# Optimization experiments

Hardware: AMD Instinct MI355X
Metric: run time of the kernel (lower is better)

Reference implementation:

```python
import jax, jax.numpy as jnp
import numpy as np

GROUPS = 4
PPG = 16  # kv_channels // groups = 64 // 4
Q_CH = 256
KV_CH = 64


def setup_inputs() -> dict:
    key = jax.random.key(0)
    ks = jax.random.split(key, 7)
    N, T, L = 4, 64, 64
    q = jax.random.normal(ks[0], (N, L, L, Q_CH), dtype=jnp.float32)
    kv = jax.random.normal(ks[1], (N, T, L, L, KV_CH), dtype=jnp.float32)
    # torch nn.Linear weights, stored pre-transposed so y = x @ W
    s_q = 1.0 / np.sqrt(Q_CH)
    s_kv = 1.0 / np.sqrt(KV_CH)
    Wq = jax.random.uniform(ks[2], (Q_CH, KV_CH), jnp.float32, -s_q, s_q)
    Wk = jax.random.uniform(ks[3], (KV_CH, KV_CH), jnp.float32, -s_kv, s_kv)
    Wv = jax.random.uniform(ks[4], (KV_CH, KV_CH), jnp.float32, -s_kv, s_kv)
    Wout = jax.random.uniform(ks[5], (KV_CH, Q_CH), jnp.float32, -s_kv, s_kv)
    b_out = jax.random.uniform(ks[6], (Q_CH,), jnp.float32, -s_kv, s_kv)
    return {"q": q, "kv": kv, "Wq": Wq, "Wk": Wk, "Wv": Wv, "Wout": Wout, "b_out": b_out}


def reference(q, kv, Wq, Wk, Wv, Wout, b_out):
    N, L, _, _ = q.shape
    T = kv.shape[1]
    qh = (q @ Wq).reshape(N, L, L, GROUPS, PPG)                 # nijgc
    kh = (kv @ Wk).reshape(N, T, L, L, GROUPS, PPG)             # ntijgc
    vh = (kv @ Wv).reshape(N, T, L, L, GROUPS, PPG)             # ntijgc
    scale = 1.0 / jnp.sqrt(jnp.float32(PPG))
    attn = jnp.einsum('nijgc,ntijgc->ntijg', qh, kh) * scale    # scores over T per pixel
    attn = jax.nn.softmax(attn, axis=1)
    x = jnp.einsum('ntijg,ntijgc->nijgc', attn, vh).reshape(N, L, L, KV_CH)
    return x @ Wout + b_out
```

## Files before the change

### kernel.cpp

```cpp
#include <hip/hip_runtime.h>

typedef short short8 __attribute__((ext_vector_type(8)));
typedef short short4v __attribute__((ext_vector_type(4)));
typedef float f32x4 __attribute__((ext_vector_type(4)));

__device__ __forceinline__ float bf2f(unsigned short u) {
  union { unsigned int i; float f; } v; v.i = ((unsigned int)u) << 16; return v.f;
}
__device__ __forceinline__ unsigned short f2bf(float f) {
  unsigned int x = __float_as_uint(f);
  unsigned int r = (x + 0x7fffu + ((x >> 16) & 1u)) >> 16;
  return (unsigned short)r;
}

__global__ __launch_bounds__(256) void prep_kernel(
    const float* __restrict__ Wq, const float* __restrict__ Wk,
    const float* __restrict__ Wv, const float* __restrict__ Wout,
    unsigned short* __restrict__ Afrag, unsigned short* __restrict__ WVOfrag) {
  const int b = blockIdx.x, tid = threadIdx.x;
  if (b < 256) {
    const int p = b, g = tid >> 6, d = tid & 63;
    float s = 0.f;
#pragma unroll
    for (int c = 0; c < 16; ++c)
      s += Wq[p * 64 + g * 16 + c] * Wk[d * 64 + g * 16 + c];
    s *= 0.25f;
    const int n = g * 64 + d, k = p;
    Afrag[(size_t)(k >> 5) * 8192 + n * 32 + (k & 31)] = f2bf(s);
  } else {
    const int row = b - 256, g = row >> 6, d = row & 63, q = tid;
    float s = 0.f;
#pragma unroll
    for (int c = 0; c < 16; ++c)
      s += Wv[d * 64 + g * 16 + c] * Wout[(g * 16 + c) * 256 + q];
    WVOfrag[(size_t)(row >> 5) * 8192 + q * 32 + (row & 31)] = f2bf(s);
  }
}

template <int MODE>
__global__ __launch_bounds__(256) void gemm256_kernel(
    const void* __restrict__ Xv, const unsigned short* __restrict__ Wfrag,
    void* __restrict__ Outv, const float* __restrict__ bias) {
  __shared__ unsigned short A_s[32 * 40];
  const int tid = threadIdx.x;
  const int m0 = blockIdx.x * 32;
  const int w = tid >> 6, lane = tid & 63;
  const int m_l = lane & 15, quad = lane >> 4;
  const int nt0 = (w & 1) * 8, m16 = (w >> 1) * 16;
  const int srow = tid >> 3, sc4 = (tid & 7) * 4;

  f32x4 acc[8];
#pragma unroll
  for (int i = 0; i < 8; ++i) acc[i] = (f32x4){0.f, 0.f, 0.f, 0.f};

  for (int ks = 0; ks < 8; ++ks) {
    if (MODE == 0) {
      const float* X = (const float*)Xv;
      float4 x = *(const float4*)(X + (size_t)(m0 + srow) * 256 + ks * 32 + sc4);
      short4v vv;
      vv[0] = (short)f2bf(x.x); vv[1] = (short)f2bf(x.y);
      vv[2] = (short)f2bf(x.z); vv[3] = (short)f2bf(x.w);
      *(short4v*)&A_s[srow * 40 + sc4] = vv;
    } else {
      const unsigned short* X = (const unsigned short*)Xv;
      uint2 xv = *(const uint2*)(X + (size_t)(m0 + srow) * 256 + ks * 32 + sc4);
      *(uint2*)&A_s[srow * 40 + sc4] = xv;
    }
    __syncthreads();
    short8 a = *(const short8*)&A_s[(m16 + m_l) * 40 + quad * 8];
#pragma unroll
    for (int j = 0; j < 8; ++j) {
      const unsigned short* bp =
          Wfrag + ((size_t)ks * 256 + (nt0 + j) * 16 + m_l) * 32 + quad * 8;
      short8 bfr = *(const short8*)bp;
      acc[j] = __builtin_amdgcn_mfma_f32_16x16x32_bf16(a, bfr, acc[j], 0, 0, 0);
    }
    __syncthreads();
  }
  const int row0 = m0 + m16 + quad * 4;
#pragma unroll
  for (int j = 0; j < 8; ++j) {
    const int col = (nt0 + j) * 16 + m_l;
    if (MODE == 0) {
      unsigned short* Out = (unsigned short*)Outv;
#pragma unroll
      for (int r = 0; r < 4; ++r)
        Out[(size_t)(row0 + r) * 256 + col] = f2bf(acc[j][r]);
    } else {
      float* Out = (float*)Outv;
      const float bb = bias[col];
#pragma unroll
      for (int r = 0; r < 4; ++r)
        Out[(size_t)(row0 + r) * 256 + col] = acc[j][r] + bb;
    }
  }
}

__global__ __launch_bounds__(256) void attn_kernel(
    const float* __restrict__ kv, const unsigned short* __restrict__ qk,
    unsigned short* __restrict__ yout) {
  __shared__ float kv_s[64 * 68];
  __shared__ float p2[256];
  __shared__ float yst[64 * 20];
  float* s_lds = yst;

  const int pixel = blockIdx.x;
  const int tid = threadIdx.x;
  const int t = tid >> 2, q4 = tid & 3;

  const unsigned short* qkb = qk + ((size_t)pixel << 8);
  uint4 qa[4], qb[4];
#pragma unroll
  for (int g = 0; g < 4; ++g) {
    const uint4* qp = (const uint4*)(qkb + g * 64 + q4 * 16);
    qa[g] = qp[0]; qb[g] = qp[1];
  }
  const float* kvb =
      kv + ((size_t)(pixel >> 12) << 24) + (size_t)(pixel & 4095) * 64;
  const float4* kp = (const float4*)(kvb + (size_t)t * 262144 + q4 * 16);
  float4 k0 = kp[0], k1 = kp[1], k2 = kp[2], k3 = kp[3];

  float4* ksw = (float4*)&kv_s[t * 68 + q4 * 16];
  ksw[0] = k0; ksw[1] = k1; ksw[2] = k2; ksw[3] = k3;
  const float kvr[16] = {k0.x, k0.y, k0.z, k0.w, k1.x, k1.y, k1.z, k1.w,
                         k2.x, k2.y, k2.z, k2.w, k3.x, k3.y, k3.z, k3.w};

  float sg[4];
#pragma unroll
  for (int g = 0; g < 4; ++g) {
    const unsigned int uu[8] = {qa[g].x, qa[g].y, qa[g].z, qa[g].w,
                                qb[g].x, qb[g].y, qb[g].z, qb[g].w};
    float acc = 0.f;
#pragma unroll
    for (int i = 0; i < 8; ++i) {
      acc = fmaf(kvr[2 * i],     bf2f((unsigned short)(uu[i] & 0xffffu)), acc);
      acc = fmaf(kvr[2 * i + 1], bf2f((unsigned short)(uu[i] >> 16)),     acc);
    }
    sg[g] = acc;
  }
#pragma unroll
  for (int g = 0; g < 4; ++g) {
    float v = sg[g];
    v += __shfl_xor(v, 1);
    v += __shfl_xor(v, 2);
    sg[g] = v;
  }
  s_lds[q4 * 65 + t] = sg[q4];
  __syncthreads();

  {
    const int g = tid >> 6, tt = tid & 63;
    float x = s_lds[g * 65 + tt];
    float m = x;
#pragma unroll
    for (int o = 32; o > 0; o >>= 1) m = fmaxf(m, __shfl_xor(m, o));
    float e = __expf(x - m);
    float ssum = e;
#pragma unroll
    for (int o = 32; o > 0; o >>= 1) ssum += __shfl_xor(ssum, o);
    p2[tt * 4 + g] = e / ssum;
  }
  __syncthreads();

  {
    const int tq = tid >> 6, d = tid & 63;
    float a0 = 0.f, a1 = 0.f, a2 = 0.f, a3 = 0.f;
#pragma unroll
    for (int i = 0; i < 16; ++i) {
      const int t2 = tq * 16 + i;
      const float kvv = kv_s[t2 * 68 + d];
      const float4 pv = *(const float4*)&p2[t2 * 4];
      a0 = fmaf(pv.x, kvv, a0);
      a1 = fmaf(pv.y, kvv, a1);
      a2 = fmaf(pv.z, kvv, a2);
      a3 = fmaf(pv.w, kvv, a3);
    }
    __syncthreads();
    yst[d * 20 + 0 + tq] = a0;
    yst[d * 20 + 4 + tq] = a1;
    yst[d * 20 + 8 + tq] = a2;
    yst[d * 20 + 12 + tq] = a3;
  }
  __syncthreads();

  {
    const int g = tid >> 6, d = tid & 63;
    const float4 v = *(const float4*)&yst[d * 20 + g * 4];
    yout[((size_t)pixel << 8) + g * 64 + d] = f2bf(v.x + v.y + v.z + v.w);
  }
}

extern "C" void kernel_launch(void* const* d_in, const int* in_sizes, int n_in,
                              void* d_out, int out_size, void* d_ws,
                              size_t ws_size, hipStream_t stream) {
  const float* q    = (const float*)d_in[0];
  const float* kv   = (const float*)d_in[1];
  const float* Wq   = (const float*)d_in[2];
  const float* Wk   = (const float*)d_in[3];
  const float* Wv   = (const float*)d_in[4];
  const float* Wout = (const float*)d_in[5];
  const float* bout = (const float*)d_in[6];

  unsigned short* ws      = (unsigned short*)d_ws;
  unsigned short* Afrag   = ws;
  unsigned short* WVOfrag = ws + 65536;
  unsigned short* qk_ws   = ws + 131072;
  unsigned short* y_ws    = ws + 131072 + 4194304;

  hipLaunchKernelGGL(prep_kernel, dim3(512), dim3(256), 0, stream,
                     Wq, Wk, Wv, Wout, Afrag, WVOfrag);
  hipLaunchKernelGGL((gemm256_kernel<0>), dim3(512), dim3(256), 0, stream,
                     (const void*)q, Afrag, (void*)qk_ws, (const float*)nullptr);
  hipLaunchKernelGGL(attn_kernel, dim3(16384), dim3(256), 0, stream,
                     kv, qk_ws, y_ws);
  hipLaunchKernelGGL((gemm256_kernel<1>), dim3(512), dim3(256), 0, stream,
                     (const void*)y_ws, WVOfrag, d_out, bout);
}
```

Measured before the change: 422.6 us.

## Restructure attention into per-row blocks with streamed async KV loads and online softmax

The attention kernel now runs one workgroup per (batch, row) of 64 pixels instead of one per pixel. Each thread owns one pixel-group pair and loops over T. KV tiles are streamed into a triple-buffered LDS ring with global_load_lds async copies, and scores and the weighted sum are accumulated in a single pass. The goal is contiguous, overlapped KV reads and far fewer tiny workgroups with their repeated barriers. The cost is only 256 workgroups at one wave group per CU, heavy register use, and an exp taken without subtracting the max, which can overflow for large scores.

```diff
diff --git a/kernel.cpp b/kernel.cpp
--- a/kernel.cpp
+++ b/kernel.cpp
@@ -11,6 +11,12 @@
   unsigned int x = __float_as_uint(f);
   unsigned int r = (x + 0x7fffu + ((x >> 16) & 1u)) >> 16;
   return (unsigned short)r;
+}
+
+typedef __attribute__((address_space(1))) void* gas_t;
+typedef __attribute__((address_space(3))) void* las_t;
+__device__ __forceinline__ void async16(const float* g, float* l) {
+  __builtin_amdgcn_global_load_lds((gas_t)g, (las_t)l, 16, 0, 0);
 }
 
 __global__ __launch_bounds__(256) void prep_kernel(
@@ -96,98 +102,103 @@
   }
 }
 
-__global__ __launch_bounds__(256) void attn_kernel(
+__global__ __launch_bounds__(256, 1) void attn_kernel(
     const float* __restrict__ kv, const unsigned short* __restrict__ qk,
     unsigned short* __restrict__ yout) {
-  __shared__ float kv_s[64 * 68];
-  __shared__ float p2[256];
-  __shared__ float yst[64 * 20];
-  float* s_lds = yst;
-
-  const int pixel = blockIdx.x;
+  __shared__ float kvbuf[3][4096];
+  __shared__ unsigned short qk_s[16384];
+
   const int tid = threadIdx.x;
-  const int t = tid >> 2, q4 = tid & 3;
-
-  const unsigned short* qkb = qk + ((size_t)pixel << 8);
-  uint4 qa[4], qb[4];
-#pragma unroll
-  for (int g = 0; g < 4; ++g) {
-    const uint4* qp = (const uint4*)(qkb + g * 64 + q4 * 16);
-    qa[g] = qp[0]; qb[g] = qp[1];
-  }
-  const float* kvb =
-      kv + ((size_t)(pixel >> 12) << 24) + (size_t)(pixel & 4095) * 64;
-  const float4* kp = (const float4*)(kvb + (size_t)t * 262144 + q4 * 16);
-  float4 k0 = kp[0], k1 = kp[1], k2 = kp[2], k3 = kp[3];
-
-  float4* ksw = (float4*)&kv_s[t * 68 + q4 * 16];
-  ksw[0] = k0; ksw[1] = k1; ksw[2] = k2; ksw[3] = k3;
-  const float kvr[16] = {k0.x, k0.y, k0.z, k0.w, k1.x, k1.y, k1.z, k1.w,
-                         k2.x, k2.y, k2.z, k2.w, k3.x, k3.y, k3.z, k3.w};
-
-  float sg[4];
-#pragma unroll
-  for (int g = 0; g < 4; ++g) {
-    const unsigned int uu[8] = {qa[g].x, qa[g].y, qa[g].z, qa[g].w,
-                                qb[g].x, qb[g].y, qb[g].z, qb[g].w};
-    float acc = 0.f;
-#pragma unroll
-    for (int i = 0; i < 8; ++i) {
-      acc = fmaf(kvr[2 * i],     bf2f((unsigned short)(uu[i] & 0xffffu)), acc);
-      acc = fmaf(kvr[2 * i + 1], bf2f((unsigned short)(uu[i] >> 16)),     acc);
-    }
-    sg[g] = acc;
-  }
-#pragma unroll
-  for (int g = 0; g < 4; ++g) {
-    float v = sg[g];
-    v += __shfl_xor(v, 1);
-    v += __shfl_xor(v, 2);
-    sg[g] = v;
-  }
-  s_lds[q4 * 65 + t] = sg[q4];
+  const int wgid = blockIdx.x;
+  const int n = wgid >> 6, i = wgid & 63;
+  const int j = tid >> 2, g = tid & 3;
+  const int w = tid >> 6, lane = tid & 63;
+
+  const float* kvblk = kv + ((size_t)n << 24) + ((size_t)i << 12);
+  const int loff = w * 1024 + lane * 4;
+
+#pragma unroll
+  for (int q = 0; q < 4; ++q)
+    async16(kvblk + loff + q * 256, &kvbuf[0][loff + q * 256]);
+#pragma unroll
+  for (int q = 0; q < 4; ++q)
+    async16(kvblk + (1 << 18) + loff + q * 256, &kvbuf[1][loff + q * 256]);
+
+  const unsigned short* qkb = qk + ((size_t)wgid << 14);
+#pragma unroll
+  for (int it = 0; it < 8; ++it)
+    *(uint4*)&qk_s[(it * 256 + tid) * 8] =
+        *(const uint4*)(qkb + (it * 256 + tid) * 8);
   __syncthreads();
 
-  {
-    const int g = tid >> 6, tt = tid & 63;
-    float x = s_lds[g * 65 + tt];
-    float m = x;
-#pragma unroll
-    for (int o = 32; o > 0; o >>= 1) m = fmaxf(m, __shfl_xor(m, o));
-    float e = __expf(x - m);
-    float ssum = e;
-#pragma unroll
-    for (int o = 32; o > 0; o >>= 1) ssum += __shfl_xor(ssum, o);
-    p2[tt * 4 + g] = e / ssum;
+  float qf[64];
+#pragma unroll
+  for (int c = 0; c < 16; ++c) {
+    const int rot = (c + j) & 15;
+    uint2 u = *(const uint2*)&qk_s[j * 256 + g * 64 + rot * 4];
+    qf[4 * c + 0] = bf2f((unsigned short)(u.x & 0xffffu));
+    qf[4 * c + 1] = bf2f((unsigned short)(u.x >> 16));
+    qf[4 * c + 2] = bf2f((unsigned short)(u.y & 0xffffu));
+    qf[4 * c + 3] = bf2f((unsigned short)(u.y >> 16));
+  }
+
+  float yac[64];
+#pragma unroll
+  for (int c = 0; c < 64; ++c) yac[c] = 0.f;
+  float lsum = 0.f;
+
+  int b = 0, ib = 2;
+  for (int t = 0; t < 64; ++t) {
+    if (t >= 1) __syncthreads();
+    if (t + 2 < 64) {
+      const float* src = kvblk + ((size_t)(t + 2) << 18) + loff;
+      float* dst = &kvbuf[ib][loff];
+#pragma unroll
+      for (int q = 0; q < 4; ++q) async16(src + q * 256, dst + q * 256);
+    }
+    const float* row = &kvbuf[b][j * 64];
+    float s = 0.f;
+    float4 cv[16];
+#pragma unroll
+    for (int c = 0; c < 16; ++c) {
+      const int rot = (c + j) & 15;
+      cv[c] = *(const float4*)(row + rot * 4);
+      s = fmaf(cv[c].x, qf[4 * c + 0], s);
+      s = fmaf(cv[c].y, qf[4 * c + 1], s);
+      s = fmaf(cv[c].z, qf[4 * c + 2], s);
+      s = fmaf(cv[c].w, qf[4 * c + 3], s);
+    }
+    const float p = __expf(s);
+    lsum += p;
+#pragma unroll
+    for (int c = 0; c < 16; ++c) {
+      yac[4 * c + 0] = fmaf(p, cv[c].x, yac[4 * c + 0]);
+      yac[4 * c + 1] = fmaf(p, cv[c].y, yac[4 * c + 1]);
+      yac[4 * c + 2] = fmaf(p, cv[c].z, yac[4 * c + 2]);
+      yac[4 * c + 3] = fmaf(p, cv[c].w, yac[4 * c + 3]);
+    }
+    b = (b == 2) ? 0 : b + 1;
+    ib = (ib == 2) ? 0 : ib + 1;
+  }
+
+  const float inv = 1.f / lsum;
+  unsigned int* yst = (unsigned int*)qk_s;
+#pragma unroll
+  for (int c = 0; c < 16; ++c) {
+    const int rot = (c + j) & 15;
+    uint2 pk;
+    pk.x = (unsigned int)f2bf(yac[4 * c + 0] * inv) |
+           ((unsigned int)f2bf(yac[4 * c + 1] * inv) << 16);
+    pk.y = (unsigned int)f2bf(yac[4 * c + 2] * inv) |
+           ((unsigned int)f2bf(yac[4 * c + 3] * inv) << 16);
+    *(uint2*)&yst[j * 128 + g * 32 + rot * 2] = pk;
   }
   __syncthreads();
-
-  {
-    const int tq = tid >> 6, d = tid & 63;
-    float a0 = 0.f, a1 = 0.f, a2 = 0.f, a3 = 0.f;
-#pragma unroll
-    for (int i = 0; i < 16; ++i) {
-      const int t2 = tq * 16 + i;
-      const float kvv = kv_s[t2 * 68 + d];
-      const float4 pv = *(const float4*)&p2[t2 * 4];
-      a0 = fmaf(pv.x, kvv, a0);
-      a1 = fmaf(pv.y, kvv, a1);
-      a2 = fmaf(pv.z, kvv, a2);
-      a3 = fmaf(pv.w, kvv, a3);
-    }
-    __syncthreads();
-    yst[d * 20 + 0 + tq] = a0;
-    yst[d * 20 + 4 + tq] = a1;
-    yst[d * 20 + 8 + tq] = a2;
-    yst[d * 20 + 12 + tq] = a3;
-  }
-  __syncthreads();
-
-  {
-    const int g = tid >> 6, d = tid & 63;
-    const float4 v = *(const float4*)&yst[d * 20 + g * 4];
-    yout[((size_t)pixel << 8) + g * 64 + d] = f2bf(v.x + v.y + v.z + v.w);
-  }
+  unsigned short* yo = yout + ((size_t)wgid << 14);
+  const uint4* srcv = (const uint4*)qk_s;
+#pragma unroll
+  for (int it = 0; it < 8; ++it)
+    *(uint4*)(yo + (it * 256 + tid) * 8) = srcv[it * 256 + tid];
 }
 
 extern "C" void kernel_launch(void* const* d_in, const int* in_sizes, int n_in,
@@ -211,7 +222,7 @@
                      Wq, Wk, Wv, Wout, Afrag, WVOfrag);
   hipLaunchKernelGGL((gemm256_kernel<0>), dim3(512), dim3(256), 0, stream,
                      (const void*)q, Afrag, (void*)qk_ws, (const float*)nullptr);
-  hipLaunchKernelGGL(attn_kernel, dim3(16384), dim3(256), 0, stream,
+  hipLaunchKernelGGL(attn_kernel, dim3(256), dim3(256), 0, stream,
                      kv, qk_ws, y_ws);
   hipLaunchKernelGGL((gemm256_kernel<1>), dim3(512), dim3(256), 0, stream,
                      (const void*)y_ws, WVOfrag, d_out, bout);
```

After: 436.0 us. 1.03x slower.
